# Optimization experiments

Measured on AMD Instinct MI355X. Metric: run time of the kernel, lower is better.

## Reference

```python
import jax, jax.numpy as jnp
import numpy as np

N, E, EP, D = 50000, 600000, 200000, 128
L = 3  # gnn layers


def _w(k, shape):
    # Kaiming-ish init: scale by 1/sqrt(fan_in)
    return jax.random.normal(k, shape, jnp.float32) / jnp.sqrt(jnp.float32(shape[-2]))


def setup_inputs() -> dict:
    key = jax.random.key(0)
    ks = jax.random.split(key, 20)
    x = jax.random.normal(ks[0], (N, D), jnp.float32)
    edge_attr = jax.random.normal(ks[1], (E, 1), jnp.float32)
    edge_index = jax.random.randint(ks[2], (2, E), 0, N, jnp.int64)
    predict_edge_index = jax.random.randint(ks[3], (2, EP), 0, N, jnp.int64)
    return {
        "x": x,
        "edge_attr": edge_attr,
        "edge_index": edge_index,
        "predict_edge_index": predict_edge_index,
        # SAGEConv params per layer: out = lin_l(mean_aggr) + lin_r(x); lin_r has no bias
        "Wl": _w(ks[4], (L, D, D)),
        "bl": jnp.zeros((L, D), jnp.float32),
        "Wr": _w(ks[5], (L, D, D)),
        # edge update MLPs: layer0 in=2D+1, layers 1..L-1 in=3D
        "euW0": _w(ks[6], (2 * D + 1, D)),
        "euB0": jnp.zeros((D,), jnp.float32),
        "euW": _w(ks[7], (L - 1, 3 * D, D)),
        "euB": jnp.zeros((L - 1, D), jnp.float32),
        # node post MLP
        "pW1": _w(ks[8], (D, D)), "pb1": jnp.zeros((D,), jnp.float32),
        "pW2": _w(ks[9], (D, D)), "pb2": jnp.zeros((D,), jnp.float32),
        # edge predict MLP (predict_mode=0: concat of two node embeddings)
        "qW1": _w(ks[10], (2 * D, D)), "qb1": jnp.zeros((D,), jnp.float32),
        "qW2": _w(ks[11], (D, 1)), "qb2": jnp.zeros((1,), jnp.float32),
    }


def reference(x, edge_attr, edge_index, predict_edge_index,
              Wl, bl, Wr, euW0, euB0, euW, euB,
              pW1, pb1, pW2, pb2, qW1, qb1, qW2, qb2):
    # dropout p=0.0 / eval mode -> identity
    src, dst = edge_index[0], edge_index[1]
    n = x.shape[0]
    deg = jax.ops.segment_sum(jnp.ones(src.shape, jnp.float32), dst, num_segments=n)
    deg = jnp.maximum(deg, 1.0)[:, None]
    for l in range(L):
        # SAGEConv: mean-aggregate source features at destinations
        aggr = jax.ops.segment_sum(x[src], dst, num_segments=n) / deg
        x = jax.nn.relu(aggr @ Wl[l] + bl[l] + x @ Wr[l])
        # edge update: gather endpoints, concat with edge_attr, Linear+ReLU (+outer relu no-op)
        cat = jnp.concatenate([x[src], x[dst], edge_attr], axis=-1)
        if l == 0:
            edge_attr = jax.nn.relu(cat @ euW0 + euB0)
        else:
            edge_attr = jax.nn.relu(cat @ euW[l - 1] + euB[l - 1])
    # node post MLP
    x = jax.nn.relu(x @ pW1 + pb1) @ pW2 + pb2
    # predict_mode=0: gather pair endpoints and score
    xi = x[predict_edge_index[0]]
    xj = x[predict_edge_index[1]]
    h = jnp.concatenate([xi, xj], axis=-1)
    y = jax.nn.relu(h @ qW1 + qb1) @ qW2 + qb2  # [EP, 1]
    return y
```

## Files before the change

kernel.cpp:

```cpp
#include <hip/hip_runtime.h>


typedef __attribute__((ext_vector_type(8))) short bf16x8;
typedef __attribute__((ext_vector_type(4))) float f32x4;

__device__ __forceinline__ unsigned short f2bf(float x) {
  unsigned u = __float_as_uint(x);
  u += 0x7fffu + ((u >> 16) & 1u);
  return (unsigned short)(u >> 16);
}
__device__ __forceinline__ float bf2f(unsigned short h) {
  return __uint_as_float(((unsigned)h) << 16);
}
__device__ __forceinline__ float lo16f(unsigned u) { return __uint_as_float(u << 16); }
__device__ __forceinline__ float hi16f(unsigned u) { return __uint_as_float(u & 0xffff0000u); }

__global__ void k_count(const int* __restrict__ dst, int* __restrict__ cnt, int E) {
  int i = blockIdx.x * blockDim.x + threadIdx.x;
  if (i < E) atomicAdd(&cnt[dst[i]], 1);
}

__global__ void k_scan1(const int* __restrict__ cnt, int* __restrict__ rs,
                        float* __restrict__ degf, int* __restrict__ bsum, int n) {
  __shared__ int wsum[16];
  __shared__ int wpre[16];
  const int tid = threadIdx.x;
  const int lane = tid & 63;
  const int wv = tid >> 6;
  int i = blockIdx.x * 1024 + tid;
  int v = (i < n) ? cnt[i] : 0;
  int s = v;
#pragma unroll
  for (int off = 1; off < 64; off <<= 1) {
    int t = __shfl_up(s, off);
    if (lane >= off) s += t;
  }
  if (lane == 63) wsum[wv] = s;
  __syncthreads();
  if (tid < 16) {
    int t = wsum[tid];
    int ss = t;
#pragma unroll
    for (int off = 1; off < 16; off <<= 1) {
      int u = __shfl_up(ss, off);
      if (tid >= off) ss += u;
    }
    wpre[tid] = ss - t;
  }
  __syncthreads();
  if (i < n) {
    rs[i] = s - v + wpre[wv];
    degf[i] = (float)(v > 0 ? v : 1);
  }
  if (tid == 1023) bsum[blockIdx.x] = wpre[15] + wsum[15];
}

__global__ void k_scan2(const int* __restrict__ bsum, int* __restrict__ boff,
                        int* __restrict__ rs_n, int nb) {
  int tid = threadIdx.x;
  int v = (tid < nb) ? bsum[tid] : 0;
  int s = v;
#pragma unroll
  for (int off = 1; off < 64; off <<= 1) {
    int t = __shfl_up(s, off);
    if (tid >= off) s += t;
  }
  if (tid < nb) boff[tid] = s - v;
  if (tid == 63) rs_n[0] = s;
}

__global__ void k_scan3(int* __restrict__ rs, const int* __restrict__ boff,
                        int* __restrict__ cursor, int n) {
  int i = blockIdx.x * blockDim.x + threadIdx.x;
  if (i < n) {
    int r = rs[i] + boff[i >> 10];
    rs[i] = r;
    cursor[i] = r;
  }
}

__global__ void k_scatter(const int* __restrict__ src, const int* __restrict__ dst,
                          int* __restrict__ cursor, int* __restrict__ csr, int E) {
  int i = blockIdx.x * blockDim.x + threadIdx.x;
  if (i < E) {
    int p = atomicAdd(&cursor[dst[i]], 1);
    csr[p] = src[i];
  }
}

__global__ void k_split(const float* __restrict__ x, unsigned* __restrict__ X,
                        long n2) {
  long g = (long)blockIdx.x * blockDim.x + threadIdx.x;
  if (g >= n2) return;
  float2 v = ((const float2*)x)[g];
  unsigned short hx = f2bf(v.x), hy = f2bf(v.y);
  unsigned short lx = f2bf(v.x - bf2f(hx)), ly = f2bf(v.y - bf2f(hy));
  long row = g >> 6, p = g & 63;
  X[row * 128 + p] = (unsigned)hx | ((unsigned)hy << 16);
  X[row * 128 + 64 + p] = (unsigned)lx | ((unsigned)ly << 16);
}

__global__ void k_packW(const float* __restrict__ W, unsigned short* __restrict__ hi,
                        unsigned short* __restrict__ lo, int nmat) {
  int gid = blockIdx.x * blockDim.x + threadIdx.x;
  if (gid >= nmat * 2048) return;
  int lane = gid & 63;
  int f = (gid >> 6) & 31;
  int mat = gid >> 11;
  int nt = f >> 2, ks = f & 3;
  int n = nt * 16 + (lane & 15);
  int k0 = ks * 32 + 8 * (lane >> 4);
  const float* Wm = W + (size_t)mat * 16384;
  size_t dst = (size_t)gid * 8;
#pragma unroll
  for (int r = 0; r < 8; ++r) {
    float w = Wm[(size_t)(k0 + r) * 128 + n];
    unsigned short h = f2bf(w);
    hi[dst + r] = h;
    lo[dst + r] = f2bf(w - bf2f(h));
  }
}

__global__ void k_aggr(const unsigned short* __restrict__ X,
                       const int* __restrict__ csr, const int* __restrict__ rs,
                       const float* __restrict__ degf,
                       unsigned short* __restrict__ Bd, int n) {
  int gid = blockIdx.x * blockDim.x + threadIdx.x;
  int wid = gid >> 6, lane = gid & 63;
  if (wid >= n) return;
  int s = rs[wid], e = rs[wid + 1];
  const int h = lane >> 4;
  const int o16 = (lane & 15) * 8;
  float a0 = 0.f, a1 = 0.f, a2 = 0.f, a3 = 0.f;
  float a4 = 0.f, a5 = 0.f, a6 = 0.f, a7 = 0.f;
  int j = s;
  for (; j + 7 < e; j += 8) {
    int n0 = csr[j + h];
    int n1 = csr[j + 4 + h];
    uint4 v0 = *(const uint4*)(X + (size_t)n0 * 256 + o16);
    uint4 v1 = *(const uint4*)(X + (size_t)n1 * 256 + o16);
    a0 += lo16f(v0.x) + lo16f(v1.x);
    a1 += hi16f(v0.x) + hi16f(v1.x);
    a2 += lo16f(v0.y) + lo16f(v1.y);
    a3 += hi16f(v0.y) + hi16f(v1.y);
    a4 += lo16f(v0.z) + lo16f(v1.z);
    a5 += hi16f(v0.z) + hi16f(v1.z);
    a6 += lo16f(v0.w) + lo16f(v1.w);
    a7 += hi16f(v0.w) + hi16f(v1.w);
  }
  for (; j < e; j += 4) {
    int idx = j + h;
    bool ok = idx < e;
    int nn = ok ? csr[idx] : 0;
    uint4 v = *(const uint4*)(X + (size_t)nn * 256 + o16);
    float m = ok ? 1.f : 0.f;
    a0 += m * lo16f(v.x); a1 += m * hi16f(v.x);
    a2 += m * lo16f(v.y); a3 += m * hi16f(v.y);
    a4 += m * lo16f(v.z); a5 += m * hi16f(v.z);
    a6 += m * lo16f(v.w); a7 += m * hi16f(v.w);
  }
  a0 += __shfl_xor(a0, 16); a1 += __shfl_xor(a1, 16);
  a2 += __shfl_xor(a2, 16); a3 += __shfl_xor(a3, 16);
  a4 += __shfl_xor(a4, 16); a5 += __shfl_xor(a5, 16);
  a6 += __shfl_xor(a6, 16); a7 += __shfl_xor(a7, 16);
  a0 += __shfl_xor(a0, 32); a1 += __shfl_xor(a1, 32);
  a2 += __shfl_xor(a2, 32); a3 += __shfl_xor(a3, 32);
  a4 += __shfl_xor(a4, 32); a5 += __shfl_xor(a5, 32);
  a6 += __shfl_xor(a6, 32); a7 += __shfl_xor(a7, 32);
  if (lane < 16) {
    float inv = 1.0f / degf[wid];
    unsigned short h0 = f2bf(a0 * inv), h1 = f2bf(a1 * inv);
    unsigned short h2 = f2bf(a2 * inv), h3 = f2bf(a3 * inv);
    unsigned short h4 = f2bf(a4 * inv), h5 = f2bf(a5 * inv);
    unsigned short h6 = f2bf(a6 * inv), h7 = f2bf(a7 * inv);
    uint4 oh;
    oh.x = (unsigned)h0 | ((unsigned)h1 << 16);
    oh.y = (unsigned)h2 | ((unsigned)h3 << 16);
    oh.z = (unsigned)h4 | ((unsigned)h5 << 16);
    oh.w = (unsigned)h6 | ((unsigned)h7 << 16);
    *(uint4*)(Bd + (size_t)wid * 128 + o16) = oh;
  }
}

template <int NPHASE, int EPI, int A0DENSE>
__global__ __launch_bounds__(256) void k_gemm(
    const unsigned short* __restrict__ A0, const unsigned short* __restrict__ A1,
    const unsigned short* __restrict__ W0h, const unsigned short* __restrict__ W0l,
    const unsigned short* __restrict__ W1h, const unsigned short* __restrict__ W1l,
    const float* __restrict__ bias, unsigned short* __restrict__ O, int nrows) {
  __shared__ unsigned short smem[8 * 4096];
  unsigned short* smh = smem;
  unsigned short* sml = smem + 8 * 2048;

  const int tid = threadIdx.x;
  const int lane = tid & 63;
  const int wv = tid >> 6;
  const long row0 = ((long)blockIdx.x * 4 + wv) * 32;
  const bool active = row0 < nrows;
  const int kgrp = (lane >> 4) * 8;

  long arow[2];
#pragma unroll
  for (int rs = 0; rs < 2; ++rs) {
    long r = row0 + rs * 16 + (lane & 15);
    arow[rs] = (r < nrows) ? r : (long)(nrows - 1);
  }

  f32x4 zero = {0.f, 0.f, 0.f, 0.f};
  f32x4 acc[2][8];
#pragma unroll
  for (int rs = 0; rs < 2; ++rs)
#pragma unroll
    for (int t = 0; t < 8; ++t) acc[rs][t] = zero;

#pragma unroll
  for (int p = 0; p < NPHASE; ++p) {
    const bool dense = (p == 0) && A0DENSE;
    const unsigned short* A = p ? A1 : A0;
    const unsigned short* Wh = p ? W1h : W0h;
    const unsigned short* Wl_ = p ? W1l : W0l;
    if (p) __syncthreads();
    for (int t = tid; t < 8 * 256; t += 256) {
      ((uint4*)smh)[t] = ((const uint4*)Wh)[t];
      ((uint4*)sml)[t] = ((const uint4*)Wl_)[t];
    }
    __syncthreads();
    if (active) {
#pragma unroll
      for (int ks = 0; ks < 4; ++ks) {
        bf16x8 a_h[2], a_l[2];
#pragma unroll
        for (int rs = 0; rs < 2; ++rs) {
          if (dense) {
            a_h[rs] = *(const bf16x8*)(A + arow[rs] * 128 + ks * 32 + kgrp);
          } else {
            a_h[rs] = *(const bf16x8*)(A + arow[rs] * 256 + ks * 32 + kgrp);
            a_l[rs] = *(const bf16x8*)(A + arow[rs] * 256 + 128 + ks * 32 + kgrp);
          }
        }
#pragma unroll
        for (int nt = 0; nt < 8; ++nt) {
          const bf16x8 b_h = *(const bf16x8*)(smh + (nt * 4 + ks) * 512 + lane * 8);
          const bf16x8 b_l = *(const bf16x8*)(sml + (nt * 4 + ks) * 512 + lane * 8);
#pragma unroll
          for (int rs = 0; rs < 2; ++rs) {
            acc[rs][nt] = __builtin_amdgcn_mfma_f32_16x16x32_bf16(b_h, a_h[rs], acc[rs][nt], 0, 0, 0);
            if (!dense)
              acc[rs][nt] = __builtin_amdgcn_mfma_f32_16x16x32_bf16(b_h, a_l[rs], acc[rs][nt], 0, 0, 0);
            acc[rs][nt] = __builtin_amdgcn_mfma_f32_16x16x32_bf16(b_l, a_h[rs], acc[rs][nt], 0, 0, 0);
          }
        }
      }
    }
  }
  if (!active) return;

  const int cq = (lane >> 4) * 4;
#pragma unroll
  for (int rs = 0; rs < 2; ++rs) {
    const long row = row0 + rs * 16 + (lane & 15);
    if (row >= nrows) continue;
#pragma unroll
    for (int nt = 0; nt < 8; ++nt) {
      const int col = nt * 16 + cq;
      float4 bv = *(const float4*)(bias + col);
      float v0 = acc[rs][nt][0] + bv.x;
      float v1 = acc[rs][nt][1] + bv.y;
      float v2 = acc[rs][nt][2] + bv.z;
      float v3 = acc[rs][nt][3] + bv.w;
      if (EPI == 0) {
        v0 = fmaxf(v0, 0.f); v1 = fmaxf(v1, 0.f);
        v2 = fmaxf(v2, 0.f); v3 = fmaxf(v3, 0.f);
      }
      unsigned short h0 = f2bf(v0), h1 = f2bf(v1), h2 = f2bf(v2), h3 = f2bf(v3);
      uint2 oh;
      oh.x = (unsigned)h0 | ((unsigned)h1 << 16);
      oh.y = (unsigned)h2 | ((unsigned)h3 << 16);
      if (EPI == 2) {
        *(uint2*)(O + row * 128 + col) = oh;
      } else {
        uint2 ol;
        ol.x = (unsigned)f2bf(v0 - bf2f(h0)) | ((unsigned)f2bf(v1 - bf2f(h1)) << 16);
        ol.y = (unsigned)f2bf(v2 - bf2f(h2)) | ((unsigned)f2bf(v3 - bf2f(h3)) << 16);
        *(uint2*)(O + row * 256 + col) = oh;
        *(uint2*)(O + row * 256 + 128 + col) = ol;
      }
    }
  }
}

__global__ __launch_bounds__(256) void k_pair(
    const unsigned short* __restrict__ u, const unsigned short* __restrict__ v,
    const int* __restrict__ ps, const int* __restrict__ pd,
    const float* __restrict__ qW2, const float* __restrict__ qb2,
    float* __restrict__ out, int EP) {
  int gid = blockIdx.x * blockDim.x + threadIdx.x;
  long wid = gid >> 6;
  int lane = gid & 63;
  int sub = lane & 15, g = lane >> 4;
  long base = wid * 8;
  if (base >= EP) return;
  float4 q0 = *(const float4*)(qW2 + sub * 8);
  float4 q1 = *(const float4*)(qW2 + sub * 8 + 4);
  float qb = qb2[0];

  long p0 = base + g;
  long p1 = base + 4 + g;
  long c0 = (p0 < EP) ? p0 : (EP - 1);
  long c1 = (p1 < EP) ? p1 : (EP - 1);
  int i0 = ps[c0], j0 = pd[c0];
  int i1 = ps[c1], j1 = pd[c1];
  uint4 a0 = *(const uint4*)(u + (size_t)i0 * 128 + sub * 8);
  uint4 b0 = *(const uint4*)(v + (size_t)j0 * 128 + sub * 8);
  uint4 a1 = *(const uint4*)(u + (size_t)i1 * 128 + sub * 8);
  uint4 b1 = *(const uint4*)(v + (size_t)j1 * 128 + sub * 8);

  float s0, s1;
  {
    float t;
    t = fmaxf(lo16f(a0.x) + lo16f(b0.x), 0.f) * q0.x;
    t = fmaf(fmaxf(hi16f(a0.x) + hi16f(b0.x), 0.f), q0.y, t);
    t = fmaf(fmaxf(lo16f(a0.y) + lo16f(b0.y), 0.f), q0.z, t);
    t = fmaf(fmaxf(hi16f(a0.y) + hi16f(b0.y), 0.f), q0.w, t);
    t = fmaf(fmaxf(lo16f(a0.z) + lo16f(b0.z), 0.f), q1.x, t);
    t = fmaf(fmaxf(hi16f(a0.z) + hi16f(b0.z), 0.f), q1.y, t);
    t = fmaf(fmaxf(lo16f(a0.w) + lo16f(b0.w), 0.f), q1.z, t);
    t = fmaf(fmaxf(hi16f(a0.w) + hi16f(b0.w), 0.f), q1.w, t);
    s0 = t;
    t = fmaxf(lo16f(a1.x) + lo16f(b1.x), 0.f) * q0.x;
    t = fmaf(fmaxf(hi16f(a1.x) + hi16f(b1.x), 0.f), q0.y, t);
    t = fmaf(fmaxf(lo16f(a1.y) + lo16f(b1.y), 0.f), q0.z, t);
    t = fmaf(fmaxf(hi16f(a1.y) + hi16f(b1.y), 0.f), q0.w, t);
    t = fmaf(fmaxf(lo16f(a1.z) + lo16f(b1.z), 0.f), q1.x, t);
    t = fmaf(fmaxf(hi16f(a1.z) + hi16f(b1.z), 0.f), q1.y, t);
    t = fmaf(fmaxf(lo16f(a1.w) + lo16f(b1.w), 0.f), q1.z, t);
    t = fmaf(fmaxf(hi16f(a1.w) + hi16f(b1.w), 0.f), q1.w, t);
    s1 = t;
  }
#pragma unroll
  for (int m = 1; m < 16; m <<= 1) {
    s0 += __shfl_xor(s0, m);
    s1 += __shfl_xor(s1, m);
  }
  if (sub == 0) {
    if (p0 < EP) out[p0] = s0 + qb;
    if (p1 < EP) out[p1] = s1 + qb;
  }
}

extern "C" void kernel_launch(void* const* d_in, const int* in_sizes, int n_in,
                              void* d_out, int out_size, void* d_ws, size_t ws_size,
                              hipStream_t stream) {
  const float* x_in = (const float*)d_in[0];
  const int* ei = (const int*)d_in[2];
  const int* pe = (const int*)d_in[3];
  const float* Wl = (const float*)d_in[4];
  const float* bl = (const float*)d_in[5];
  const float* Wr = (const float*)d_in[6];
  const float* pW1 = (const float*)d_in[11];
  const float* pb1 = (const float*)d_in[12];
  const float* pW2 = (const float*)d_in[13];
  const float* pb2 = (const float*)d_in[14];
  const float* qW1 = (const float*)d_in[15];
  const float* qb1 = (const float*)d_in[16];
  const float* qW2 = (const float*)d_in[17];
  const float* qb2 = (const float*)d_in[18];

  const int N = in_sizes[0] / 128;
  const int E = in_sizes[2] / 2;
  const int EP = in_sizes[3] / 2;
  const int* e_src = ei;
  const int* e_dst = ei + E;
  const int* p_src = pe;
  const int* p_dst = pe + EP;

  char* ws = (char*)d_ws;
  size_t off = 0;
  auto alloc = [&](size_t bytes) {
    void* p = ws + off;
    off += (bytes + 511) & ~(size_t)511;
    return p;
  };
  unsigned short* X = (unsigned short*)alloc((size_t)N * 256 * 2);
  unsigned short* B = (unsigned short*)alloc((size_t)N * 256 * 2);
  int* deg_i = (int*)alloc((size_t)N * 4);
  int* rs = (int*)alloc((size_t)(N + 1) * 4);
  int* cursor = (int*)alloc((size_t)N * 4);
  float* degf = (float*)alloc((size_t)N * 4);
  int* csr = (int*)alloc((size_t)E * 4);
  int* bsum = (int*)alloc(64 * 4);
  int* boff = (int*)alloc(64 * 4);
  unsigned short* Whi = (unsigned short*)alloc((size_t)10 * 16384 * 2);
  unsigned short* Wlo = (unsigned short*)alloc((size_t)10 * 16384 * 2);
  float* biasuv = (float*)alloc(256 * 4);

  const size_t MS = 16384;
  const int nb = (N + 1023) / 1024;

  hipMemsetAsync(deg_i, 0, (size_t)N * 4, stream);
  hipMemcpyAsync(biasuv, qb1, 128 * 4, hipMemcpyDeviceToDevice, stream);
  hipMemsetAsync(biasuv + 128, 0, 128 * 4, stream);

  k_packW<<<(3 * 2048 + 255) / 256, 256, 0, stream>>>(Wl, Whi + 0 * MS, Wlo + 0 * MS, 3);
  k_packW<<<(3 * 2048 + 255) / 256, 256, 0, stream>>>(Wr, Whi + 3 * MS, Wlo + 3 * MS, 3);
  k_packW<<<(2048 + 255) / 256, 256, 0, stream>>>(pW1, Whi + 6 * MS, Wlo + 6 * MS, 1);
  k_packW<<<(2048 + 255) / 256, 256, 0, stream>>>(pW2, Whi + 7 * MS, Wlo + 7 * MS, 1);
  k_packW<<<(2 * 2048 + 255) / 256, 256, 0, stream>>>(qW1, Whi + 8 * MS, Wlo + 8 * MS, 2);

  long n2 = (long)N * 64;
  k_split<<<(int)((n2 + 255) / 256), 256, 0, stream>>>(x_in, (unsigned*)X, n2);

  k_count<<<(E + 255) / 256, 256, 0, stream>>>(e_dst, deg_i, E);
  k_scan1<<<nb, 1024, 0, stream>>>(deg_i, rs, degf, bsum, N);
  k_scan2<<<1, 64, 0, stream>>>(bsum, boff, rs + N, nb);
  k_scan3<<<(N + 255) / 256, 256, 0, stream>>>(rs, boff, cursor, N);
  k_scatter<<<(E + 255) / 256, 256, 0, stream>>>(e_src, e_dst, cursor, csr, E);

  const int gmm = (N + 127) / 128;
  const int agblocks = (N + 3) / 4;
  for (int l = 0; l < 3; ++l) {
    k_aggr<<<agblocks, 256, 0, stream>>>(X, csr, rs, degf, B, N);
    k_gemm<2, 0, 1><<<gmm, 256, 0, stream>>>(
        B, X, Whi + (size_t)l * MS, Wlo + (size_t)l * MS,
        Whi + (size_t)(3 + l) * MS, Wlo + (size_t)(3 + l) * MS,
        bl + (size_t)l * 128, X, N);
  }
  k_gemm<1, 0, 0><<<gmm, 256, 0, stream>>>(
      X, nullptr, Whi + 6 * MS, Wlo + 6 * MS, nullptr, nullptr, pb1, B, N);
  k_gemm<1, 1, 0><<<gmm, 256, 0, stream>>>(
      B, nullptr, Whi + 7 * MS, Wlo + 7 * MS, nullptr, nullptr, pb2, X, N);
  unsigned short* u = B;
  unsigned short* v = B + (size_t)N * 128;
  k_gemm<1, 2, 0><<<gmm, 256, 0, stream>>>(
      X, nullptr, Whi + 8 * MS, Wlo + 8 * MS, nullptr, nullptr, biasuv, u, N);
  k_gemm<1, 2, 0><<<gmm, 256, 0, stream>>>(
      X, nullptr, Whi + 9 * MS, Wlo + 9 * MS, nullptr, nullptr, biasuv + 128, v, N);
  k_pair<<<(EP + 31) / 32, 256, 0, stream>>>(u, v, p_src, p_dst, qW2, qb2,
                                             (float*)d_out, EP);
}
```

Before: 316.1 us.

## Prefetch GEMM operands via direct-to-LDS loads and merge setup kernels

The GEMM kernel now loads weights with global_load_lds straight into shared memory and preloads all A fragments for both phases into registers before the first barrier, so global latency overlaps the weight staging. Separately, the five weight-pack launches become one kernel, the scan2 step folds into scan3, and the bias memcpy/memset pair becomes a tiny kernel, cutting launch count. Holding all A fragments in registers raises register pressure and may lower occupancy.

```diff
diff --git a/kernel.cpp b/kernel.cpp
--- a/kernel.cpp
+++ b/kernel.cpp
@@ -14,6 +14,12 @@
 }
 __device__ __forceinline__ float lo16f(unsigned u) { return __uint_as_float(u << 16); }
 __device__ __forceinline__ float hi16f(unsigned u) { return __uint_as_float(u & 0xffff0000u); }
+
+__device__ __forceinline__ void gload_lds16(const void* g, void* l) {
+  __builtin_amdgcn_global_load_lds(
+      (const __attribute__((address_space(1))) unsigned int*)g,
+      (__attribute__((address_space(3))) unsigned int*)l, 16, 0, 0);
+}
 
 __global__ void k_count(const int* __restrict__ dst, int* __restrict__ cnt, int E) {
   int i = blockIdx.x * blockDim.x + threadIdx.x;
@@ -55,28 +61,30 @@
   if (tid == 1023) bsum[blockIdx.x] = wpre[15] + wsum[15];
 }
 
-__global__ void k_scan2(const int* __restrict__ bsum, int* __restrict__ boff,
-                        int* __restrict__ rs_n, int nb) {
+__global__ void k_scan3(int* __restrict__ rs, const int* __restrict__ bsum,
+                        int* __restrict__ cursor, int n, int nb) {
+  __shared__ int boff_s[64];
+  __shared__ int total_s;
   int tid = threadIdx.x;
-  int v = (tid < nb) ? bsum[tid] : 0;
-  int s = v;
-#pragma unroll
-  for (int off = 1; off < 64; off <<= 1) {
-    int t = __shfl_up(s, off);
-    if (tid >= off) s += t;
-  }
-  if (tid < nb) boff[tid] = s - v;
-  if (tid == 63) rs_n[0] = s;
-}
-
-__global__ void k_scan3(int* __restrict__ rs, const int* __restrict__ boff,
-                        int* __restrict__ cursor, int n) {
-  int i = blockIdx.x * blockDim.x + threadIdx.x;
+  if (tid < 64) {
+    int v = (tid < nb) ? bsum[tid] : 0;
+    int s = v;
+#pragma unroll
+    for (int off = 1; off < 64; off <<= 1) {
+      int t = __shfl_up(s, off);
+      if (tid >= off) s += t;
+    }
+    boff_s[tid] = s - v;
+    if (tid == 63) total_s = s;
+  }
+  __syncthreads();
+  int i = blockIdx.x * blockDim.x + tid;
   if (i < n) {
-    int r = rs[i] + boff[i >> 10];
+    int r = rs[i] + boff_s[i >> 10];
     rs[i] = r;
     cursor[i] = r;
   }
+  if (blockIdx.x == 0 && tid == 0) rs[n] = total_s;
 }
 
 __global__ void k_scatter(const int* __restrict__ src, const int* __restrict__ dst,
@@ -100,25 +108,38 @@
   X[row * 128 + 64 + p] = (unsigned)lx | ((unsigned)ly << 16);
 }
 
-__global__ void k_packW(const float* __restrict__ W, unsigned short* __restrict__ hi,
-                        unsigned short* __restrict__ lo, int nmat) {
+__global__ void k_packAll(const float* __restrict__ Wl, const float* __restrict__ Wr,
+                          const float* __restrict__ pW1, const float* __restrict__ pW2,
+                          const float* __restrict__ qW1,
+                          unsigned short* __restrict__ hi,
+                          unsigned short* __restrict__ lo) {
   int gid = blockIdx.x * blockDim.x + threadIdx.x;
-  if (gid >= nmat * 2048) return;
+  if (gid >= 10 * 2048) return;
+  int mat = gid >> 11;
+  const float* Wm;
+  if (mat < 3) Wm = Wl + (size_t)mat * 16384;
+  else if (mat < 6) Wm = Wr + (size_t)(mat - 3) * 16384;
+  else if (mat == 6) Wm = pW1;
+  else if (mat == 7) Wm = pW2;
+  else Wm = qW1 + (size_t)(mat - 8) * 16384;
   int lane = gid & 63;
   int f = (gid >> 6) & 31;
-  int mat = gid >> 11;
   int nt = f >> 2, ks = f & 3;
-  int n = nt * 16 + (lane & 15);
+  int nn = nt * 16 + (lane & 15);
   int k0 = ks * 32 + 8 * (lane >> 4);
-  const float* Wm = W + (size_t)mat * 16384;
   size_t dst = (size_t)gid * 8;
 #pragma unroll
   for (int r = 0; r < 8; ++r) {
-    float w = Wm[(size_t)(k0 + r) * 128 + n];
+    float w = Wm[(size_t)(k0 + r) * 128 + nn];
     unsigned short h = f2bf(w);
     hi[dst + r] = h;
     lo[dst + r] = f2bf(w - bf2f(h));
   }
+}
+
+__global__ void k_biasuv(const float* __restrict__ qb1, float* __restrict__ b) {
+  int i = threadIdx.x;
+  b[i] = (i < 128) ? qb1[i] : 0.f;
 }
 
 __global__ void k_aggr(const unsigned short* __restrict__ X,
@@ -206,6 +227,32 @@
     arow[rs] = (r < nrows) ? r : (long)(nrows - 1);
   }
 
+#pragma unroll
+  for (int k = 0; k < 8; ++k) {
+    int t = tid + k * 256;
+    gload_lds16((const uint4*)W0h + t, (uint4*)smh + t);
+    gload_lds16((const uint4*)W0l + t, (uint4*)sml + t);
+  }
+
+  bf16x8 a0h[2][4], a0l[2][4], a1h[2][4], a1l[2][4];
+  if (active) {
+#pragma unroll
+    for (int rs = 0; rs < 2; ++rs)
+#pragma unroll
+      for (int ks = 0; ks < 4; ++ks) {
+        if (A0DENSE) {
+          a0h[rs][ks] = *(const bf16x8*)(A0 + arow[rs] * 128 + ks * 32 + kgrp);
+        } else {
+          a0h[rs][ks] = *(const bf16x8*)(A0 + arow[rs] * 256 + ks * 32 + kgrp);
+          a0l[rs][ks] = *(const bf16x8*)(A0 + arow[rs] * 256 + 128 + ks * 32 + kgrp);
+        }
+        if (NPHASE == 2) {
+          a1h[rs][ks] = *(const bf16x8*)(A1 + arow[rs] * 256 + ks * 32 + kgrp);
+          a1l[rs][ks] = *(const bf16x8*)(A1 + arow[rs] * 256 + 128 + ks * 32 + kgrp);
+        }
+      }
+  }
+
   f32x4 zero = {0.f, 0.f, 0.f, 0.f};
   f32x4 acc[2][8];
 #pragma unroll
@@ -213,41 +260,47 @@
 #pragma unroll
     for (int t = 0; t < 8; ++t) acc[rs][t] = zero;
 
-#pragma unroll
-  for (int p = 0; p < NPHASE; ++p) {
-    const bool dense = (p == 0) && A0DENSE;
-    const unsigned short* A = p ? A1 : A0;
-    const unsigned short* Wh = p ? W1h : W0h;
-    const unsigned short* Wl_ = p ? W1l : W0l;
-    if (p) __syncthreads();
-    for (int t = tid; t < 8 * 256; t += 256) {
-      ((uint4*)smh)[t] = ((const uint4*)Wh)[t];
-      ((uint4*)sml)[t] = ((const uint4*)Wl_)[t];
+  __syncthreads();
+
+  if (active) {
+#pragma unroll
+    for (int ks = 0; ks < 4; ++ks) {
+#pragma unroll
+      for (int nt = 0; nt < 8; ++nt) {
+        const bf16x8 b_h = *(const bf16x8*)(smh + (nt * 4 + ks) * 512 + lane * 8);
+        const bf16x8 b_l = *(const bf16x8*)(sml + (nt * 4 + ks) * 512 + lane * 8);
+#pragma unroll
+        for (int rs = 0; rs < 2; ++rs) {
+          acc[rs][nt] = __builtin_amdgcn_mfma_f32_16x16x32_bf16(b_h, a0h[rs][ks], acc[rs][nt], 0, 0, 0);
+          if (!A0DENSE)
+            acc[rs][nt] = __builtin_amdgcn_mfma_f32_16x16x32_bf16(b_h, a0l[rs][ks], acc[rs][nt], 0, 0, 0);
+          acc[rs][nt] = __builtin_amdgcn_mfma_f32_16x16x32_bf16(b_l, a0h[rs][ks], acc[rs][nt], 0, 0, 0);
+        }
+      }
+    }
+  }
+
+  if (NPHASE == 2) {
+    __syncthreads();
+#pragma unroll
+    for (int k = 0; k < 8; ++k) {
+      int t = tid + k * 256;
+      gload_lds16((const uint4*)W1h + t, (uint4*)smh + t);
+      gload_lds16((const uint4*)W1l + t, (uint4*)sml + t);
     }
     __syncthreads();
     if (active) {
 #pragma unroll
       for (int ks = 0; ks < 4; ++ks) {
-        bf16x8 a_h[2], a_l[2];
-#pragma unroll
-        for (int rs = 0; rs < 2; ++rs) {
-          if (dense) {
-            a_h[rs] = *(const bf16x8*)(A + arow[rs] * 128 + ks * 32 + kgrp);
-          } else {
-            a_h[rs] = *(const bf16x8*)(A + arow[rs] * 256 + ks * 32 + kgrp);
-            a_l[rs] = *(const bf16x8*)(A + arow[rs] * 256 + 128 + ks * 32 + kgrp);
-          }
-        }
 #pragma unroll
         for (int nt = 0; nt < 8; ++nt) {
           const bf16x8 b_h = *(const bf16x8*)(smh + (nt * 4 + ks) * 512 + lane * 8);
           const bf16x8 b_l = *(const bf16x8*)(sml + (nt * 4 + ks) * 512 + lane * 8);
 #pragma unroll
           for (int rs = 0; rs < 2; ++rs) {
-            acc[rs][nt] = __builtin_amdgcn_mfma_f32_16x16x32_bf16(b_h, a_h[rs], acc[rs][nt], 0, 0, 0);
-            if (!dense)
-              acc[rs][nt] = __builtin_amdgcn_mfma_f32_16x16x32_bf16(b_h, a_l[rs], acc[rs][nt], 0, 0, 0);
-            acc[rs][nt] = __builtin_amdgcn_mfma_f32_16x16x32_bf16(b_l, a_h[rs], acc[rs][nt], 0, 0, 0);
+            acc[rs][nt] = __builtin_amdgcn_mfma_f32_16x16x32_bf16(b_h, a1h[rs][ks], acc[rs][nt], 0, 0, 0);
+            acc[rs][nt] = __builtin_amdgcn_mfma_f32_16x16x32_bf16(b_h, a1l[rs][ks], acc[rs][nt], 0, 0, 0);
+            acc[rs][nt] = __builtin_amdgcn_mfma_f32_16x16x32_bf16(b_l, a1h[rs][ks], acc[rs][nt], 0, 0, 0);
           }
         }
       }
@@ -389,7 +442,6 @@
   float* degf = (float*)alloc((size_t)N * 4);
   int* csr = (int*)alloc((size_t)E * 4);
   int* bsum = (int*)alloc(64 * 4);
-  int* boff = (int*)alloc(64 * 4);
   unsigned short* Whi = (unsigned short*)alloc((size_t)10 * 16384 * 2);
   unsigned short* Wlo = (unsigned short*)alloc((size_t)10 * 16384 * 2);
   float* biasuv = (float*)alloc(256 * 4);
@@ -398,22 +450,17 @@
   const int nb = (N + 1023) / 1024;
 
   hipMemsetAsync(deg_i, 0, (size_t)N * 4, stream);
-  hipMemcpyAsync(biasuv, qb1, 128 * 4, hipMemcpyDeviceToDevice, stream);
-  hipMemsetAsync(biasuv + 128, 0, 128 * 4, stream);
-
-  k_packW<<<(3 * 2048 + 255) / 256, 256, 0, stream>>>(Wl, Whi + 0 * MS, Wlo + 0 * MS, 3);
-  k_packW<<<(3 * 2048 + 255) / 256, 256, 0, stream>>>(Wr, Whi + 3 * MS, Wlo + 3 * MS, 3);
-  k_packW<<<(2048 + 255) / 256, 256, 0, stream>>>(pW1, Whi + 6 * MS, Wlo + 6 * MS, 1);
-  k_packW<<<(2048 + 255) / 256, 256, 0, stream>>>(pW2, Whi + 7 * MS, Wlo + 7 * MS, 1);
-  k_packW<<<(2 * 2048 + 255) / 256, 256, 0, stream>>>(qW1, Whi + 8 * MS, Wlo + 8 * MS, 2);
+  k_biasuv<<<1, 256, 0, stream>>>(qb1, biasuv);
+
+  k_packAll<<<(10 * 2048 + 255) / 256, 256, 0, stream>>>(Wl, Wr, pW1, pW2, qW1,
+                                                         Whi, Wlo);
 
   long n2 = (long)N * 64;
   k_split<<<(int)((n2 + 255) / 256), 256, 0, stream>>>(x_in, (unsigned*)X, n2);
 
   k_count<<<(E + 255) / 256, 256, 0, stream>>>(e_dst, deg_i, E);
   k_scan1<<<nb, 1024, 0, stream>>>(deg_i, rs, degf, bsum, N);
-  k_scan2<<<1, 64, 0, stream>>>(bsum, boff, rs + N, nb);
-  k_scan3<<<(N + 255) / 256, 256, 0, stream>>>(rs, boff, cursor, N);
+  k_scan3<<<(N + 255) / 256, 256, 0, stream>>>(rs, bsum, cursor, N, nb);
   k_scatter<<<(E + 255) / 256, 256, 0, stream>>>(e_src, e_dst, cursor, csr, E);
 
   const int gmm = (N + 127) / 128;
```

Measured after the change: 320.1 us. About the same (+1.3%).
